# Kernel optimization log

Measured on AMD Instinct MI355X. Metric: run time of the kernel, lower is better.

Reference implementation:

```python
import jax, jax.numpy as jnp
import numpy as np

D_MODEL = 1024
NUM_HEADS = 16
D_K = D_MODEL // NUM_HEADS


def setup_inputs() -> dict:
    key = jax.random.key(0)
    kx, kq, kk, kv, ko = jax.random.split(key, 5)
    B, S = 4, 2048
    scale = 1.0 / np.sqrt(D_MODEL)
    return {
        "x": jax.random.normal(kx, (B, S, D_MODEL), dtype=jnp.float32),
        "W_q": jax.random.normal(kq, (D_MODEL, D_MODEL), dtype=jnp.float32) * scale,
        "W_k": jax.random.normal(kk, (D_MODEL, D_MODEL), dtype=jnp.float32) * scale,
        "W_v": jax.random.normal(kv, (D_MODEL, D_MODEL), dtype=jnp.float32) * scale,
        "W_o": jax.random.normal(ko, (D_MODEL, D_MODEL), dtype=jnp.float32) * scale,
    }


def reference(x, W_q, W_k, W_v, W_o):
    B, S, _ = x.shape
    # torch Linear: y = x @ W.T
    def proj(W):
        return (x @ W.T).reshape(B, S, NUM_HEADS, D_K).transpose(0, 2, 1, 3)  # [B,H,S,Dk]
    Q, K, V = proj(W_q), proj(W_k), proj(W_v)
    scores = jnp.einsum("bhqd,bhkd->bhqk", Q, K) / jnp.sqrt(jnp.float32(D_K))
    attn = jax.nn.softmax(scores, axis=-1)
    out = jnp.einsum("bhqk,bhkd->bhqd", attn, V)  # [B,H,S,Dk]
    out = out.transpose(0, 2, 1, 3).reshape(B, S, D_MODEL)
    return out @ W_o.T
```

## Files before the change

### kernel.cpp

```cpp
#include <hip/hip_runtime.h>
#include <hip/hip_bf16.h>

typedef unsigned short u16;
typedef __bf16 bf16x8 __attribute__((ext_vector_type(8)));
typedef float f32x4 __attribute__((ext_vector_type(4)));

#define DEV static __device__ __forceinline__

DEV u16 f2b(float f){
  union { float f; unsigned u; } v; v.f = f;
  unsigned r = (v.u + 0x7FFFu + ((v.u >> 16) & 1u)) >> 16;
  return (u16)r;
}

DEV unsigned pack2(float lo, float hi){
  __hip_bfloat162 h = __float22bfloat162_rn(float2{lo, hi});
  union { __hip_bfloat162 h; unsigned u; } c; c.h = h;
  return c.u;
}

DEV unsigned pack_trunc(float lo, float hi){
  union { float f; unsigned u; } a, b; a.f = lo; b.f = hi;
  return __builtin_amdgcn_perm(b.u, a.u, 0x07060302u);
}

DEV void gload16(const void* g, void* l){
  __builtin_amdgcn_global_load_lds((const __attribute__((address_space(1))) void*)g,
                                   (__attribute__((address_space(3))) void*)l, 16, 0, 0);
}

DEV f32x4 mfma16(bf16x8 a, bf16x8 b, f32x4 c){
  return __builtin_amdgcn_mfma_f32_16x16x32_bf16(a, b, c, 0, 0, 0);
}

__global__ void cvt_all(const float* __restrict__ x,
                        const float* __restrict__ w0, const float* __restrict__ w1,
                        const float* __restrict__ w2, const float* __restrict__ w3,
                        u16* __restrict__ xb,
                        u16* __restrict__ o0, u16* __restrict__ o1,
                        u16* __restrict__ o2, u16* __restrict__ o3){
  const int bid = blockIdx.x;
  const float* s; u16* d; int i;
  if (bid < 8192){
    s = x; d = xb; i = bid * 256 + threadIdx.x;
  } else {
    int r = (bid - 8192) >> 10;
    i = ((bid - 8192) & 1023) * 256 + threadIdx.x;
    s = (r == 0) ? w0 : (r == 1) ? w1 : (r == 2) ? w2 : w3;
    d = (r == 0) ? o0 : (r == 1) ? o1 : (r == 2) ? o2 : o3;
  }
  float4 v = reinterpret_cast<const float4*>(s)[i];
  ushort4 o;
  o.x = f2b(v.x); o.y = f2b(v.y); o.z = f2b(v.z); o.w = f2b(v.w);
  reinterpret_cast<ushort4*>(d)[i] = o;
}

__global__ __launch_bounds__(256, 2)
void gemm_qkv(const u16* __restrict__ A, const u16* __restrict__ B,
              u16* __restrict__ Qb, u16* __restrict__ Kb, u16* __restrict__ Vtb){
  __shared__ __align__(16) u16 lsA[128*64];
  __shared__ __align__(16) u16 lsB[128*64];
  const int tid  = threadIdx.x;
  const int lane = tid & 63, wid = tid >> 6;
  const int g = lane >> 4, c15 = lane & 15;
  const int m0 = blockIdx.x * 128, n0 = blockIdx.y * 128;
  const int wm = (wid >> 1) * 64, wn = (wid & 1) * 64;
  const f32x4 vzero = {0.f, 0.f, 0.f, 0.f};

  f32x4 acc[4][4];
#pragma unroll
  for (int mi = 0; mi < 4; ++mi)
#pragma unroll
    for (int ni = 0; ni < 4; ++ni) acc[mi][ni] = vzero;

  for (int kt = 0; kt < 16; ++kt){
    __syncthreads();
#pragma unroll
    for (int i = 0; i < 4; ++i){
      int c = i * 256 + tid;
      int row = c >> 3, gc = (c & 7) ^ (row & 7);
      gload16(A + ((size_t)(m0 + row) << 10) + (kt << 6) + (gc << 3), lsA + (size_t)c * 8);
    }
#pragma unroll
    for (int i = 0; i < 4; ++i){
      int c = i * 256 + tid;
      int row = c >> 3, gc = (c & 7) ^ (row & 7);
      gload16(B + ((size_t)(n0 + row) << 10) + (kt << 6) + (gc << 3), lsB + (size_t)c * 8);
    }
    __syncthreads();

    bf16x8 af[4][2], bf[4][2];
#pragma unroll
    for (int mi = 0; mi < 4; ++mi)
#pragma unroll
      for (int kk = 0; kk < 2; ++kk){
        int ra = wm + mi * 16 + c15;
        af[mi][kk] = *reinterpret_cast<const bf16x8*>(lsA + ra * 64 + ((((kk << 2) + g) ^ (ra & 7)) << 3));
        int rb = wn + mi * 16 + c15;
        bf[mi][kk] = *reinterpret_cast<const bf16x8*>(lsB + rb * 64 + ((((kk << 2) + g) ^ (rb & 7)) << 3));
      }
#pragma unroll
    for (int mi = 0; mi < 4; ++mi)
#pragma unroll
      for (int ni = 0; ni < 4; ++ni){
        acc[mi][ni] = mfma16(af[mi][0], bf[ni][0], acc[mi][ni]);
        acc[mi][ni] = mfma16(af[mi][1], bf[ni][1], acc[mi][ni]);
      }
  }

  const int reg = n0 >> 10;
#pragma unroll
  for (int mi = 0; mi < 4; ++mi)
#pragma unroll
    for (int ni = 0; ni < 4; ++ni){
      int mrow = m0 + wm + mi * 16 + g * 4;
      int ncolL = (n0 + wn + ni * 16 + c15) & 1023;
      int b = mrow >> 11, s = mrow & 2047;
      int h = ncolL >> 6, dk = ncolL & 63;
      if (reg < 2){
        const float sc = (reg == 0) ? 0.18033688011112042f : 1.0f;
        u16* dst = (reg == 0 ? Qb : Kb) + (((size_t)(b * 16 + h) * 2048 + s) << 6) + dk;
#pragma unroll
        for (int r = 0; r < 4; ++r) dst[(size_t)r << 6] = f2b(acc[mi][ni][r] * sc);
      } else {
        ushort4 o;
        o.x = f2b(acc[mi][ni][0]); o.y = f2b(acc[mi][ni][1]);
        o.z = f2b(acc[mi][ni][2]); o.w = f2b(acc[mi][ni][3]);
        int sl = s & 63;
        int np = (sl & 0x20) | ((sl & 0x0C) << 1) | ((sl & 0x10) >> 2);
        *reinterpret_cast<ushort4*>(Vtb + (((size_t)(b * 16 + h) * 64 + dk) << 11) + (s & ~63) + np) = o;
      }
    }
}

__global__ __launch_bounds__(256, 2)
void gemm_out(const u16* __restrict__ A, const u16* __restrict__ B, float* __restrict__ Out){
  __shared__ __align__(16) u16 lsA[128*64];
  __shared__ __align__(16) u16 lsB[128*64];
  const int tid  = threadIdx.x;
  const int lane = tid & 63, wid = tid >> 6;
  const int g = lane >> 4, c15 = lane & 15;
  const int m0 = blockIdx.x * 128, n0 = blockIdx.y * 128;
  const int wm = (wid >> 1) * 64, wn = (wid & 1) * 64;
  const f32x4 vzero = {0.f, 0.f, 0.f, 0.f};

  f32x4 acc[4][4];
#pragma unroll
  for (int mi = 0; mi < 4; ++mi)
#pragma unroll
    for (int ni = 0; ni < 4; ++ni) acc[mi][ni] = vzero;

  for (int kt = 0; kt < 16; ++kt){
    __syncthreads();
#pragma unroll
    for (int i = 0; i < 4; ++i){
      int c = i * 256 + tid;
      int row = c >> 3, gc = (c & 7) ^ (row & 7);
      int b = m0 >> 11, s = (m0 & 2047) + row;
      gload16(A + (((size_t)(b * 16 + kt) * 2048 + s) << 6) + (gc << 3), lsA + (size_t)c * 8);
    }
#pragma unroll
    for (int i = 0; i < 4; ++i){
      int c = i * 256 + tid;
      int row = c >> 3, gc = (c & 7) ^ (row & 7);
      gload16(B + ((size_t)(n0 + row) << 10) + (kt << 6) + (gc << 3), lsB + (size_t)c * 8);
    }
    __syncthreads();

    bf16x8 af[4][2], bf[4][2];
#pragma unroll
    for (int mi = 0; mi < 4; ++mi)
#pragma unroll
      for (int kk = 0; kk < 2; ++kk){
        int ra = wm + mi * 16 + c15;
        af[mi][kk] = *reinterpret_cast<const bf16x8*>(lsA + ra * 64 + ((((kk << 2) + g) ^ (ra & 7)) << 3));
        int rb = wn + mi * 16 + c15;
        bf[mi][kk] = *reinterpret_cast<const bf16x8*>(lsB + rb * 64 + ((((kk << 2) + g) ^ (rb & 7)) << 3));
      }
#pragma unroll
    for (int mi = 0; mi < 4; ++mi)
#pragma unroll
      for (int ni = 0; ni < 4; ++ni){
        acc[mi][ni] = mfma16(af[mi][0], bf[ni][0], acc[mi][ni]);
        acc[mi][ni] = mfma16(af[mi][1], bf[ni][1], acc[mi][ni]);
      }
  }

#pragma unroll
  for (int mi = 0; mi < 4; ++mi)
#pragma unroll
    for (int ni = 0; ni < 4; ++ni){
      int mrow = m0 + wm + mi * 16 + g * 4;
      int ncol = n0 + wn + ni * 16 + c15;
      float* dst = Out + (size_t)mrow * 1024 + ncol;
#pragma unroll
      for (int r = 0; r < 4; ++r) dst[(size_t)r << 10] = acc[mi][ni][r];
    }
}

__global__ __launch_bounds__(256, 4)
void attn_kernel(const u16* __restrict__ Q, const u16* __restrict__ K,
                 const u16* __restrict__ Vt, u16* __restrict__ O){
  __shared__ __align__(16) u16 lsK[2][64*64];
  __shared__ __align__(16) u16 lsV[2][64*64];
  const int tid  = threadIdx.x;
  const int lane = tid & 63;
  const int g = lane >> 4, c15 = lane & 15;
  const int bid  = blockIdx.x;
  const int head = (bid & 7) * 8 + ((bid >> 3) >> 4);
  const int qt   = (bid >> 3) & 15;
  const size_t hb = (size_t)head << 17;
  const int q0 = qt * 128 + (tid >> 6) * 32;
  const f32x4 vzero = {0.f, 0.f, 0.f, 0.f};

#define STAGE_T(tb, tt) do {                                                        \
    _Pragma("unroll")                                                               \
    for (int i_ = 0; i_ < 2; ++i_){                                                 \
      int c_ = i_ * 256 + tid;                                                      \
      int row_ = c_ >> 3, gc_ = (c_ & 7) ^ (row_ & 7);                              \
      gload16(K  + hb + ((size_t)((tt)*64 + row_) << 6) + (gc_ << 3), lsK[tb] + (size_t)c_ * 8); \
      gload16(Vt + hb + ((size_t)row_ << 11) + (tt)*64 + (gc_ << 3),  lsV[tb] + (size_t)c_ * 8); \
    }                                                                               \
  } while (0)

  bf16x8 qf[2][2];
#pragma unroll
  for (int mi = 0; mi < 2; ++mi)
#pragma unroll
    for (int kk = 0; kk < 2; ++kk)
      qf[mi][kk] = *reinterpret_cast<const bf16x8*>(Q + hb + ((size_t)(q0 + mi*16 + c15) << 6) + kk*32 + g*8);

  union { unsigned u[4]; bf16x8 v; } ou;
  ou.u[0] = ou.u[1] = ou.u[2] = ou.u[3] = 0x3F803F80u;
  const bf16x8 ones = ou.v;

  f32x4 oaccT[2][4];
  float mrun[2], lrun[2];
#pragma unroll
  for (int mi = 0; mi < 2; ++mi){
#pragma unroll
    for (int di = 0; di < 4; ++di) oaccT[mi][di] = vzero;
    mrun[mi] = -1e30f; lrun[mi] = 0.f;
  }

  STAGE_T(0, 0);
  __syncthreads();

  for (int t = 0; t < 32; ++t){
    const int cur = t & 1;
    if (t < 31) STAGE_T(cur ^ 1, t + 1);
    const u16* bK = lsK[cur];
    const u16* bV = lsV[cur];

    bf16x8 kf[4][2];
#pragma unroll
    for (int ni = 0; ni < 4; ++ni)
#pragma unroll
      for (int kk = 0; kk < 2; ++kk){
        int row = ni*16 + c15;
        kf[ni][kk] = *reinterpret_cast<const bf16x8*>(bK + row*64 + ((((kk<<2)+g) ^ (row&7)) << 3));
      }
    f32x4 sacc[2][4];
    __builtin_amdgcn_s_setprio(1);
#pragma unroll
    for (int mi = 0; mi < 2; ++mi)
#pragma unroll
      for (int ni = 0; ni < 4; ++ni)
        sacc[mi][ni] = mfma16(kf[ni][1], qf[mi][1], mfma16(kf[ni][0], qf[mi][0], vzero));
    __builtin_amdgcn_s_setprio(0);

    bf16x8 pf[2][2];
#pragma unroll
    for (int mi = 0; mi < 2; ++mi){
      float a0 = fmaxf(fmaxf(sacc[mi][0][0], sacc[mi][0][1]), sacc[mi][0][2]);
      float a1 = fmaxf(fmaxf(sacc[mi][0][3], sacc[mi][1][0]), sacc[mi][1][1]);
      float a2 = fmaxf(fmaxf(sacc[mi][1][2], sacc[mi][1][3]), sacc[mi][2][0]);
      float a3 = fmaxf(fmaxf(sacc[mi][2][1], sacc[mi][2][2]), sacc[mi][2][3]);
      float a4 = fmaxf(fmaxf(sacc[mi][3][0], sacc[mi][3][1]), sacc[mi][3][2]);
      float b0 = fmaxf(fmaxf(a0, a1), a2);
      float b1 = fmaxf(fmaxf(a3, a4), sacc[mi][3][3]);
      float mt = fmaxf(b0, b1);
      mt = fmaxf(mt, __shfl_xor(mt, 16, 64));
      mt = fmaxf(mt, __shfl_xor(mt, 32, 64));
      if (mt > mrun[mi]){
        float f_ = __builtin_amdgcn_exp2f(mrun[mi] - mt);
        mrun[mi] = mt;
        lrun[mi] *= f_;
#pragma unroll
        for (int di = 0; di < 4; ++di) oaccT[mi][di] = oaccT[mi][di] * f_;
      }
      const float mn = mrun[mi];
#pragma unroll
      for (int kk = 0; kk < 2; ++kk){
        union { unsigned u[4]; bf16x8 v; } pu;
#pragma unroll
        for (int h2 = 0; h2 < 2; ++h2){
          const int ni = 2*kk + h2;
          float p0 = __builtin_amdgcn_exp2f(sacc[mi][ni][0] - mn);
          float p1 = __builtin_amdgcn_exp2f(sacc[mi][ni][1] - mn);
          float p2 = __builtin_amdgcn_exp2f(sacc[mi][ni][2] - mn);
          float p3 = __builtin_amdgcn_exp2f(sacc[mi][ni][3] - mn);
          pu.u[2*h2    ] = pack_trunc(p0, p1);
          pu.u[2*h2 + 1] = pack_trunc(p2, p3);
        }
        pf[mi][kk] = pu.v;
      }
    }

    bf16x8 vf[4][2];
#pragma unroll
    for (int di = 0; di < 4; ++di)
#pragma unroll
      for (int kk = 0; kk < 2; ++kk){
        int row = di*16 + c15;
        vf[di][kk] = *reinterpret_cast<const bf16x8*>(bV + row*64 + ((((kk<<2)+g) ^ (row&7)) << 3));
      }

    __builtin_amdgcn_s_setprio(1);
#pragma unroll
    for (int mi = 0; mi < 2; ++mi){
      f32x4 ls = mfma16(ones, pf[mi][0], vzero);
      ls = mfma16(ones, pf[mi][1], ls);
      lrun[mi] += ls[0];
    }
#pragma unroll
    for (int mi = 0; mi < 2; ++mi)
#pragma unroll
      for (int di = 0; di < 4; ++di){
        oaccT[mi][di] = mfma16(vf[di][0], pf[mi][0], oaccT[mi][di]);
        oaccT[mi][di] = mfma16(vf[di][1], pf[mi][1], oaccT[mi][di]);
      }
    __builtin_amdgcn_s_setprio(0);

    __syncthreads();
  }

#pragma unroll
  for (int mi = 0; mi < 2; ++mi){
    float inv = 1.f / lrun[mi];
    int q = q0 + mi*16 + c15;
#pragma unroll
    for (int di = 0; di < 4; ++di){
      unsigned lo = pack2(oaccT[mi][di][0] * inv, oaccT[mi][di][1] * inv);
      unsigned hi = pack2(oaccT[mi][di][2] * inv, oaccT[mi][di][3] * inv);
      *reinterpret_cast<uint2*>(O + hb + ((size_t)q << 6) + di*16 + g*4) = make_uint2(lo, hi);
    }
  }
#undef STAGE_T
}

extern "C" void kernel_launch(void* const* d_in, const int* in_sizes, int n_in,
                              void* d_out, int out_size, void* d_ws, size_t ws_size,
                              hipStream_t stream){
  const float* x  = (const float*)d_in[0];
  const float* wq = (const float*)d_in[1];
  const float* wk = (const float*)d_in[2];
  const float* wv = (const float*)d_in[3];
  const float* wo = (const float*)d_in[4];
  float* out = (float*)d_out;
  char* ws = (char*)d_ws;
  u16* xb  = (u16*)(ws);
  u16* wqb = (u16*)(ws + (16u << 20));
  u16* wkb = (u16*)(ws + (18u << 20));
  u16* wvb = (u16*)(ws + (20u << 20));
  u16* wob = (u16*)(ws + (22u << 20));
  u16* Qb  = (u16*)(ws + (24u << 20));
  u16* Kb  = (u16*)(ws + (40u << 20));
  u16* Vtb = (u16*)(ws + (56u << 20));
  u16* Ob  = (u16*)(ws + (72u << 20));

  cvt_all<<<12288, 256, 0, stream>>>(x, wq, wk, wv, wo, xb, wqb, wkb, wvb, wob);
  gemm_qkv<<<dim3(64, 24), 256, 0, stream>>>(xb, wqb, Qb, Kb, Vtb);
  attn_kernel<<<1024, 256, 0, stream>>>(Qb, Kb, Vtb, Ob);
  gemm_out<<<dim3(64, 8), 256, 0, stream>>>(Ob, wob, out);
}
```

Before: 177.9 us.

## Shrink attention query tile and drop LDS double buffering for higher occupancy

Each attention block now handles 64 queries instead of 128, with each wave owning 16 query rows, and the grid doubles to 2048 blocks. The K/V shared-memory tiles go from double-buffered to single-buffered, with a barrier before and after each stage, and launch bounds rise to 8 blocks per CU. The aim is to cut registers and LDS per block so more waves can hide latency. In exchange, each K/V tile is loaded from global memory twice as often, per-wave MFMA reuse of K/V fragments is halved, and the prefetch overlap is gone.

Result: slower. 292.0 us (+64.1%).

```diff
diff --git a/kernel.cpp b/kernel.cpp
--- a/kernel.cpp
+++ b/kernel.cpp
@@ -198,59 +198,49 @@
     }
 }
 
-__global__ __launch_bounds__(256, 4)
+__global__ __launch_bounds__(256, 8)
 void attn_kernel(const u16* __restrict__ Q, const u16* __restrict__ K,
                  const u16* __restrict__ Vt, u16* __restrict__ O){
-  __shared__ __align__(16) u16 lsK[2][64*64];
-  __shared__ __align__(16) u16 lsV[2][64*64];
+  __shared__ __align__(16) u16 lsK[64*64];
+  __shared__ __align__(16) u16 lsV[64*64];
   const int tid  = threadIdx.x;
   const int lane = tid & 63;
   const int g = lane >> 4, c15 = lane & 15;
   const int bid  = blockIdx.x;
-  const int head = (bid & 7) * 8 + ((bid >> 3) >> 4);
-  const int qt   = (bid >> 3) & 15;
+  const int head = (bid & 7) * 8 + ((bid >> 3) >> 5);
+  const int qt   = (bid >> 3) & 31;
   const size_t hb = (size_t)head << 17;
-  const int q0 = qt * 128 + (tid >> 6) * 32;
+  const int q0 = qt * 64 + (tid >> 6) * 16;
   const f32x4 vzero = {0.f, 0.f, 0.f, 0.f};
 
-#define STAGE_T(tb, tt) do {                                                        \
+#define STAGE_T(tt) do {                                                            \
     _Pragma("unroll")                                                               \
     for (int i_ = 0; i_ < 2; ++i_){                                                 \
       int c_ = i_ * 256 + tid;                                                      \
       int row_ = c_ >> 3, gc_ = (c_ & 7) ^ (row_ & 7);                              \
-      gload16(K  + hb + ((size_t)((tt)*64 + row_) << 6) + (gc_ << 3), lsK[tb] + (size_t)c_ * 8); \
-      gload16(Vt + hb + ((size_t)row_ << 11) + (tt)*64 + (gc_ << 3),  lsV[tb] + (size_t)c_ * 8); \
+      gload16(K  + hb + ((size_t)((tt)*64 + row_) << 6) + (gc_ << 3), lsK + (size_t)c_ * 8); \
+      gload16(Vt + hb + ((size_t)row_ << 11) + (tt)*64 + (gc_ << 3),  lsV + (size_t)c_ * 8); \
     }                                                                               \
   } while (0)
 
-  bf16x8 qf[2][2];
-#pragma unroll
-  for (int mi = 0; mi < 2; ++mi)
-#pragma unroll
-    for (int kk = 0; kk < 2; ++kk)
-      qf[mi][kk] = *reinterpret_cast<const bf16x8*>(Q + hb + ((size_t)(q0 + mi*16 + c15) << 6) + kk*32 + g*8);
+  bf16x8 qf[2];
+#pragma unroll
+  for (int kk = 0; kk < 2; ++kk)
+    qf[kk] = *reinterpret_cast<const bf16x8*>(Q + hb + ((size_t)(q0 + c15) << 6) + kk*32 + g*8);
 
   union { unsigned u[4]; bf16x8 v; } ou;
   ou.u[0] = ou.u[1] = ou.u[2] = ou.u[3] = 0x3F803F80u;
   const bf16x8 ones = ou.v;
 
-  f32x4 oaccT[2][4];
-  float mrun[2], lrun[2];
-#pragma unroll
-  for (int mi = 0; mi < 2; ++mi){
-#pragma unroll
-    for (int di = 0; di < 4; ++di) oaccT[mi][di] = vzero;
-    mrun[mi] = -1e30f; lrun[mi] = 0.f;
-  }
-
-  STAGE_T(0, 0);
-  __syncthreads();
+  f32x4 oaccT[4];
+  float mrun = -1e30f, lrun = 0.f;
+#pragma unroll
+  for (int di = 0; di < 4; ++di) oaccT[di] = vzero;
 
   for (int t = 0; t < 32; ++t){
-    const int cur = t & 1;
-    if (t < 31) STAGE_T(cur ^ 1, t + 1);
-    const u16* bK = lsK[cur];
-    const u16* bV = lsV[cur];
+    __syncthreads();
+    STAGE_T(t);
+    __syncthreads();
 
     bf16x8 kf[4][2];
 #pragma unroll
@@ -258,53 +248,48 @@
 #pragma unroll
       for (int kk = 0; kk < 2; ++kk){
         int row = ni*16 + c15;
-        kf[ni][kk] = *reinterpret_cast<const bf16x8*>(bK + row*64 + ((((kk<<2)+g) ^ (row&7)) << 3));
-      }
-    f32x4 sacc[2][4];
+        kf[ni][kk] = *reinterpret_cast<const bf16x8*>(lsK + row*64 + ((((kk<<2)+g) ^ (row&7)) << 3));
+      }
+    f32x4 sacc[4];
     __builtin_amdgcn_s_setprio(1);
 #pragma unroll
-    for (int mi = 0; mi < 2; ++mi)
-#pragma unroll
-      for (int ni = 0; ni < 4; ++ni)
-        sacc[mi][ni] = mfma16(kf[ni][1], qf[mi][1], mfma16(kf[ni][0], qf[mi][0], vzero));
+    for (int ni = 0; ni < 4; ++ni)
+      sacc[ni] = mfma16(kf[ni][1], qf[1], mfma16(kf[ni][0], qf[0], vzero));
     __builtin_amdgcn_s_setprio(0);
 
-    bf16x8 pf[2][2];
-#pragma unroll
-    for (int mi = 0; mi < 2; ++mi){
-      float a0 = fmaxf(fmaxf(sacc[mi][0][0], sacc[mi][0][1]), sacc[mi][0][2]);
-      float a1 = fmaxf(fmaxf(sacc[mi][0][3], sacc[mi][1][0]), sacc[mi][1][1]);
-      float a2 = fmaxf(fmaxf(sacc[mi][1][2], sacc[mi][1][3]), sacc[mi][2][0]);
-      float a3 = fmaxf(fmaxf(sacc[mi][2][1], sacc[mi][2][2]), sacc[mi][2][3]);
-      float a4 = fmaxf(fmaxf(sacc[mi][3][0], sacc[mi][3][1]), sacc[mi][3][2]);
-      float b0 = fmaxf(fmaxf(a0, a1), a2);
-      float b1 = fmaxf(fmaxf(a3, a4), sacc[mi][3][3]);
-      float mt = fmaxf(b0, b1);
-      mt = fmaxf(mt, __shfl_xor(mt, 16, 64));
-      mt = fmaxf(mt, __shfl_xor(mt, 32, 64));
-      if (mt > mrun[mi]){
-        float f_ = __builtin_amdgcn_exp2f(mrun[mi] - mt);
-        mrun[mi] = mt;
-        lrun[mi] *= f_;
-#pragma unroll
-        for (int di = 0; di < 4; ++di) oaccT[mi][di] = oaccT[mi][di] * f_;
-      }
-      const float mn = mrun[mi];
-#pragma unroll
-      for (int kk = 0; kk < 2; ++kk){
-        union { unsigned u[4]; bf16x8 v; } pu;
-#pragma unroll
-        for (int h2 = 0; h2 < 2; ++h2){
-          const int ni = 2*kk + h2;
-          float p0 = __builtin_amdgcn_exp2f(sacc[mi][ni][0] - mn);
-          float p1 = __builtin_amdgcn_exp2f(sacc[mi][ni][1] - mn);
-          float p2 = __builtin_amdgcn_exp2f(sacc[mi][ni][2] - mn);
-          float p3 = __builtin_amdgcn_exp2f(sacc[mi][ni][3] - mn);
-          pu.u[2*h2    ] = pack_trunc(p0, p1);
-          pu.u[2*h2 + 1] = pack_trunc(p2, p3);
-        }
-        pf[mi][kk] = pu.v;
-      }
+    float a0 = fmaxf(fmaxf(sacc[0][0], sacc[0][1]), sacc[0][2]);
+    float a1 = fmaxf(fmaxf(sacc[0][3], sacc[1][0]), sacc[1][1]);
+    float a2 = fmaxf(fmaxf(sacc[1][2], sacc[1][3]), sacc[2][0]);
+    float a3 = fmaxf(fmaxf(sacc[2][1], sacc[2][2]), sacc[2][3]);
+    float a4 = fmaxf(fmaxf(sacc[3][0], sacc[3][1]), sacc[3][2]);
+    float b0 = fmaxf(fmaxf(a0, a1), a2);
+    float b1 = fmaxf(fmaxf(a3, a4), sacc[3][3]);
+    float mt = fmaxf(b0, b1);
+    mt = fmaxf(mt, __shfl_xor(mt, 16, 64));
+    mt = fmaxf(mt, __shfl_xor(mt, 32, 64));
+    if (mt > mrun){
+      float f_ = __builtin_amdgcn_exp2f(mrun - mt);
+      mrun = mt;
+      lrun *= f_;
+#pragma unroll
+      for (int di = 0; di < 4; ++di) oaccT[di] = oaccT[di] * f_;
+    }
+    const float mn = mrun;
+    bf16x8 pf[2];
+#pragma unroll
+    for (int kk = 0; kk < 2; ++kk){
+      union { unsigned u[4]; bf16x8 v; } pu;
+#pragma unroll
+      for (int h2 = 0; h2 < 2; ++h2){
+        const int ni = 2*kk + h2;
+        float p0 = __builtin_amdgcn_exp2f(sacc[ni][0] - mn);
+        float p1 = __builtin_amdgcn_exp2f(sacc[ni][1] - mn);
+        float p2 = __builtin_amdgcn_exp2f(sacc[ni][2] - mn);
+        float p3 = __builtin_amdgcn_exp2f(sacc[ni][3] - mn);
+        pu.u[2*h2    ] = pack_trunc(p0, p1);
+        pu.u[2*h2 + 1] = pack_trunc(p2, p3);
+      }
+      pf[kk] = pu.v;
     }
 
     bf16x8 vf[4][2];
@@ -313,36 +298,30 @@
 #pragma unroll
       for (int kk = 0; kk < 2; ++kk){
         int row = di*16 + c15;
-        vf[di][kk] = *reinterpret_cast<const bf16x8*>(bV + row*64 + ((((kk<<2)+g) ^ (row&7)) << 3));
+        vf[di][kk] = *reinterpret_cast<const bf16x8*>(lsV + row*64 + ((((kk<<2)+g) ^ (row&7)) << 3));
       }
 
     __builtin_amdgcn_s_setprio(1);
-#pragma unroll
-    for (int mi = 0; mi < 2; ++mi){
-      f32x4 ls = mfma16(ones, pf[mi][0], vzero);
-      ls = mfma16(ones, pf[mi][1], ls);
-      lrun[mi] += ls[0];
-    }
-#pragma unroll
-    for (int mi = 0; mi < 2; ++mi)
-#pragma unroll
-      for (int di = 0; di < 4; ++di){
-        oaccT[mi][di] = mfma16(vf[di][0], pf[mi][0], oaccT[mi][di]);
-        oaccT[mi][di] = mfma16(vf[di][1], pf[mi][1], oaccT[mi][di]);
-      }
+    {
+      f32x4 ls = mfma16(ones, pf[0], vzero);
+      ls = mfma16(ones, pf[1], ls);
+      lrun += ls[0];
+    }
+#pragma unroll
+    for (int di = 0; di < 4; ++di){
+      oaccT[di] = mfma16(vf[di][0], pf[0], oaccT[di]);
+      oaccT[di] = mfma16(vf[di][1], pf[1], oaccT[di]);
+    }
     __builtin_amdgcn_s_setprio(0);
-
-    __syncthreads();
-  }
-
-#pragma unroll
-  for (int mi = 0; mi < 2; ++mi){
-    float inv = 1.f / lrun[mi];
-    int q = q0 + mi*16 + c15;
+  }
+
+  {
+    float inv = 1.f / lrun;
+    int q = q0 + c15;
 #pragma unroll
     for (int di = 0; di < 4; ++di){
-      unsigned lo = pack2(oaccT[mi][di][0] * inv, oaccT[mi][di][1] * inv);
-      unsigned hi = pack2(oaccT[mi][di][2] * inv, oaccT[mi][di][3] * inv);
+      unsigned lo = pack2(oaccT[di][0] * inv, oaccT[di][1] * inv);
+      unsigned hi = pack2(oaccT[di][2] * inv, oaccT[di][3] * inv);
       *reinterpret_cast<uint2*>(O + hb + ((size_t)q << 6) + di*16 + g*4) = make_uint2(lo, hi);
     }
   }
@@ -371,6 +350,6 @@
 
   cvt_all<<<12288, 256, 0, stream>>>(x, wq, wk, wv, wo, xb, wqb, wkb, wvb, wob);
   gemm_qkv<<<dim3(64, 24), 256, 0, stream>>>(xb, wqb, Qb, Kb, Vtb);
-  attn_kernel<<<1024, 256, 0, stream>>>(Qb, Kb, Vtb, Ob);
+  attn_kernel<<<2048, 256, 0, stream>>>(Qb, Kb, Vtb, Ob);
   gemm_out<<<dim3(64, 8), 256, 0, stream>>>(Ob, wob, out);
 }
```
